# Performance work log

Measured on AMD Instinct MI355X. Metric: run time of the kernel, lower is better.

## Reference

```python
import jax, jax.numpy as jnp
import numpy as np

B, N, D, H = 4, 2048, 512, 8
HD = D // H
SCALE = D ** (-0.5)  # module uses embed_dim**-0.5, not head_dim**-0.5


def setup_inputs() -> dict:
    key = jax.random.key(0)
    k1, k2, k3, k4 = jax.random.split(key, 4)
    x = jax.random.normal(k1, (B, N, D), dtype=jnp.float32)
    # qkv: Linear(D, 3D, bias=False); store as [D, 3D] (x @ W_qkv)
    w_qkv = jax.random.normal(k2, (D, 3 * D), dtype=jnp.float32) * (D ** -0.5)
    # out_proj: Linear(D, D) with bias
    w_out = jax.random.normal(k3, (D, D), dtype=jnp.float32) * (D ** -0.5)
    b_out = jax.random.normal(k4, (D,), dtype=jnp.float32) * 0.01
    return {"x": x, "w_qkv": w_qkv, "w_out": w_out, "b_out": b_out}


def reference(x, w_qkv, w_out, b_out):
    # qkv projection -> [B, N, 3, H, HD] -> split
    qkv = (x @ w_qkv).reshape(B, N, 3, H, HD)
    q = qkv[:, :, 0].transpose(0, 2, 1, 3)  # [B, H, N, HD]
    k = qkv[:, :, 1].transpose(0, 2, 1, 3)
    v = qkv[:, :, 2].transpose(0, 2, 1, 3)
    attn = jnp.einsum("bhqd,bhkd->bhqk", q, k) * SCALE  # [B, H, N, N]
    attn = jax.nn.softmax(attn, axis=-1)
    out = jnp.einsum("bhqk,bhkd->bhqd", attn, v)  # [B, H, N, HD]
    out = out.transpose(0, 2, 1, 3).reshape(B, N, D)
    return out @ w_out + b_out
```

## Files before the change

kernel.cpp:

```cpp
#include <hip/hip_runtime.h>

typedef __attribute__((ext_vector_type(4))) float f32x4;
typedef __attribute__((ext_vector_type(16))) float f32x16;
typedef __attribute__((ext_vector_type(8))) short short8;

#define DEV static __device__ __forceinline__

DEV unsigned short f2bf(float f) {
  union { float f; unsigned u; } x; x.f = f;
  unsigned r = x.u + 0x7fffu + ((x.u >> 16) & 1u);
  return (unsigned short)(r >> 16);
}

DEV float bf2f(unsigned short u) {
  union { unsigned u; float f; } x; x.u = ((unsigned)u) << 16;
  return x.f;
}

DEV f32x4 mfma16(short8 a, short8 b, f32x4 c) {
  return __builtin_amdgcn_mfma_f32_16x16x32_bf16(a, b, c, 0, 0, 0);
}

DEV f32x16 mfma32(short8 a, short8 b, f32x16 c) {
  return __builtin_amdgcn_mfma_f32_32x32x16_bf16(a, b, c, 0, 0, 0);
}

DEV void gload16(const void* g, void* l) {
  __builtin_amdgcn_global_load_lds(
      (const __attribute__((address_space(1))) void*)g,
      (__attribute__((address_space(3))) void*)l, 16, 0, 0);
}

DEV float exp2f_fast(float x) {
  float r;
  asm("v_exp_f32 %0, %1" : "=v"(r) : "v"(x));
  return r;
}

DEV unsigned cvtpk(float lo, float hi) {
  unsigned r;
  asm("v_cvt_pk_bf16_f32 %0, %1, %2" : "=v"(r) : "v"(lo), "v"(hi));
  return r;
}

DEV short8 mk8(unsigned w0, unsigned w1, unsigned w2, unsigned w3) {
  union { unsigned u[4]; short8 s; } x;
  x.u[0] = w0; x.u[1] = w1; x.u[2] = w2; x.u[3] = w3;
  return x.s;
}

DEV int swzrow(int r) { return (((r & 7) ^ ((r >> 3) & 7)) << 3); }

__global__ __launch_bounds__(256) void k_prep(
    const float* __restrict__ x, unsigned short* __restrict__ xb,
    const float* __restrict__ wq, unsigned short* __restrict__ wqT,
    const float* __restrict__ wo, unsigned short* __restrict__ woT) {
  __shared__ unsigned short T[64 * 72];
  const int blk = blockIdx.x;
  const int t = threadIdx.x;
  if (blk < 2048) {
    size_t i = (size_t)blk * 256 + t;
    const f32x4* p = (const f32x4*)(x + i * 8);
    f32x4 a = p[0], b = p[1];
    short8 r;
    r[0] = f2bf(a[0]); r[1] = f2bf(a[1]); r[2] = f2bf(a[2]); r[3] = f2bf(a[3]);
    r[4] = f2bf(b[0]); r[5] = f2bf(b[1]); r[6] = f2bf(b[2]); r[7] = f2bf(b[3]);
    *(short8*)(xb + i * 8) = r;
    return;
  }
  const float* in;
  unsigned short* out;
  int C, bx, by;
  const int R = 512;
  if (blk < 2240) {
    in = wq; out = wqT; C = 1536;
    int bb = blk - 2048; bx = bb % 24; by = bb / 24;
  } else {
    in = wo; out = woT; C = 512;
    int bb = blk - 2240; bx = bb & 7; by = bb >> 3;
  }
  int r0 = by * 64, c0 = bx * 64;
  int rr = t >> 2, seg = t & 3;
  const float* p = in + (size_t)(r0 + rr) * C + c0 + seg * 16;
#pragma unroll
  for (int q = 0; q < 4; ++q) {
    f32x4 v = *(const f32x4*)(p + q * 4);
#pragma unroll
    for (int e = 0; e < 4; ++e) T[rr * 72 + seg * 16 + q * 4 + e] = f2bf(v[e]);
  }
  __syncthreads();
  short8 o0, o1;
#pragma unroll
  for (int e = 0; e < 8; ++e) o0[e] = (short)T[(seg * 16 + e) * 72 + rr];
#pragma unroll
  for (int e = 0; e < 8; ++e) o1[e] = (short)T[(seg * 16 + 8 + e) * 72 + rr];
  unsigned short* q2 = out + (size_t)(c0 + rr) * R + r0 + seg * 16;
  *(short8*)q2 = o0;
  *(short8*)(q2 + 8) = o1;
}

template <bool F32OUT, int NT, bool WVT>
__global__ __launch_bounds__(256) void k_gemm_bt(
    const unsigned short* __restrict__ A, const unsigned short* __restrict__ Bt,
    void* __restrict__ Cp, const float* __restrict__ bias,
    unsigned short* __restrict__ vt, int M, int N, int K) {
  constexpr int NJ = NT / 32;
  constexpr int SHSZ = WVT ? (128 * 136) : (8192 + NT * 64);
  __shared__ unsigned short SH[SHSZ];
  unsigned short* Asm = SH;
  unsigned short* Bsm = SH + 8192;
  const int tid = threadIdx.x;
  const int lane = tid & 63, w = tid >> 6;
  const int wr = w >> 1, wc = w & 1;
  const int nbx = gridDim.x;
  const int cpx = (nbx * gridDim.y) >> 3;
  const int lin = blockIdx.y * nbx + blockIdx.x;
  const int swz = (lin & 7) * cpx + (lin >> 3);
  const int bm = (swz / nbx) * 128, bn = (swz % nbx) * NT;
  const int l15 = lane & 15, l4 = lane >> 4;
  f32x4 acc[4][NJ] = {};
  for (int k0 = 0; k0 < K; k0 += 64) {
    __syncthreads();
#pragma unroll
    for (int j = 0; j < 4; ++j) {
      int c = j * 256 + tid;
      gload16(A + (size_t)(bm + (c >> 3)) * K + k0 + ((c & 7) << 3),
              Asm + (size_t)(j * 256 + w * 64) * 8);
    }
#pragma unroll
    for (int j = 0; j < NJ; ++j) {
      int c = j * 256 + tid;
      gload16(Bt + (size_t)(bn + (c >> 3)) * K + k0 + ((c & 7) << 3),
              Bsm + (size_t)(j * 256 + w * 64) * 8);
    }
    __syncthreads();
#pragma unroll
    for (int kc = 0; kc < 2; ++kc) {
      short8 av[4], bv[NJ];
#pragma unroll
      for (int i = 0; i < 4; ++i)
        av[i] = *(const short8*)&Asm[(wr * 64 + i * 16 + l15) * 64 + kc * 32 + l4 * 8];
#pragma unroll
      for (int j = 0; j < NJ; ++j)
        bv[j] = *(const short8*)&Bsm[(wc * (NT / 2) + j * 16 + l15) * 64 + kc * 32 + l4 * 8];
#pragma unroll
      for (int i = 0; i < 4; ++i)
#pragma unroll
        for (int j = 0; j < NJ; ++j)
          acc[i][j] = mfma16(av[i], bv[j], acc[i][j]);
    }
  }
  if (WVT && bn >= 1024) {
    __syncthreads();
#pragma unroll
    for (int i = 0; i < 4; ++i)
#pragma unroll
      for (int j = 0; j < NJ; ++j) {
        int colL = wc * (NT / 2) + j * 16 + l15;
#pragma unroll
        for (int v = 0; v < 4; ++v)
          SH[colL * 136 + wr * 64 + i * 16 + l4 * 4 + v] = f2bf(acc[i][j][v]);
      }
    __syncthreads();
    const int vtrow = tid >> 1, half2 = tid & 1;
    const int b2 = bm >> 11, npos0 = bm & 2047;
    const int h = ((bn - 1024) >> 6) + (vtrow >> 6);
    const int hd = vtrow & 63;
    unsigned short* dst =
        vt + ((size_t)(b2 * 8 + h) * 64 + hd) * 2048 + npos0 + half2 * 64;
    const unsigned short* srcT = SH + vtrow * 136 + half2 * 64;
#pragma unroll
    for (int e = 0; e < 8; ++e)
      *(short8*)(dst + e * 8) = *(const short8*)(srcT + e * 8);
    return;
  }
#pragma unroll
  for (int i = 0; i < 4; ++i) {
#pragma unroll
    for (int j = 0; j < NJ; ++j) {
      int col = bn + wc * (NT / 2) + j * 16 + l15;
      float bb = 0.f;
      if constexpr (F32OUT) bb = bias[col];
#pragma unroll
      for (int v = 0; v < 4; ++v) {
        int row = bm + wr * 64 + i * 16 + l4 * 4 + v;
        if constexpr (F32OUT) {
          ((float*)Cp)[(size_t)row * N + col] = acc[i][j][v] + bb;
        } else {
          ((unsigned short*)Cp)[(size_t)row * N + col] = f2bf(acc[i][j][v]);
        }
      }
    }
  }
}

__global__ __launch_bounds__(512, 4) void k_attn5(const unsigned short* __restrict__ qkv,
                                                  const unsigned short* __restrict__ vtg,
                                                  unsigned short* __restrict__ O) {
  __shared__ unsigned short smem[16896];
  unsigned short* Ks0 = smem;
  unsigned short* Ks1 = smem + 4096;
  unsigned short* Vs0 = smem + 8192;
  unsigned short* Vs1 = smem + 12288;
  const int tid = threadIdx.x;
  const int lane = tid & 63, w = tid >> 6;
  const int qg = w & 3, half = w >> 2;
  const int l31 = lane & 31, hi = lane >> 5;
  const int bh = blockIdx.y, b = bh >> 3, h = bh & 7;
  const int q0 = blockIdx.x * 128 + qg * 32;
  const float CL = 0.044194173824159216f * 1.4426950408889634f;

  short8 qf[4];
  {
    const unsigned short* qp = qkv + (size_t)(b * 2048 + q0 + l31) * 1536 + h * 64;
#pragma unroll
    for (int ks = 0; ks < 4; ++ks) {
      short8 raw = *(const short8*)(qp + ks * 16 + hi * 8);
      short8 f;
#pragma unroll
      for (int e = 0; e < 8; ++e)
        f[e] = (short)f2bf(bf2f((unsigned short)raw[e]) * CL);
      qf[ks] = f;
    }
  }

  const int sr = tid >> 3, seg = tid & 7;
  const unsigned short* kg = qkv + (size_t)b * 2048 * 1536 + 512 + h * 64 + seg * 8;
  const unsigned short* vg = vtg + (size_t)bh * 64 * 2048 + seg * 8;
  const int so = sr * 64 + ((seg * 8) ^ swzrow(sr));

  *(short8*)&Ks0[so] = *(const short8*)(kg + (size_t)sr * 1536);
  *(short8*)&Vs0[so] = *(const short8*)(vg + (size_t)sr * 2048);
  __syncthreads();

  const int kxor = swzrow(half * 32 + l31);
  const int v0xor = swzrow(l31);
  const int v1xor = swzrow(32 + l31);
  const int krow = (half * 32 + l31) * 64;

  f32x16 oacc0 = {}, oacc1 = {};
  float m_run = 0.f, l_run = 0.f;
  unsigned short* kcur = Ks0; unsigned short* knxt = Ks1;
  unsigned short* vcur = Vs0; unsigned short* vnxt = Vs1;

  for (int t = 0; t < 32; ++t) {
    short8 pk, pv;
    if (t < 31) {
      int kv = (t + 1) * 64;
      pk = *(const short8*)(kg + (size_t)(kv + sr) * 1536);
      pv = *(const short8*)(vg + (size_t)sr * 2048 + kv);
    }

    f32x16 st = {};
    __builtin_amdgcn_s_setprio(1);
#pragma unroll
    for (int ks = 0; ks < 4; ++ks) {
      int col = ks * 16 + hi * 8;
      short8 kf = *(const short8*)&kcur[krow + (col ^ kxor)];
      st = mfma32(kf, qf[ks], st);
    }
    __builtin_amdgcn_s_setprio(0);

    float tm[8];
#pragma unroll
    for (int r = 0; r < 8; ++r) tm[r] = fmaxf(st[r], st[r + 8]);
    float pm = fmaxf(fmaxf(fmaxf(tm[0], tm[1]), fmaxf(tm[2], tm[3])),
                     fmaxf(fmaxf(tm[4], tm[5]), fmaxf(tm[6], tm[7])));
    pm = fmaxf(pm, __shfl_xor(pm, 32));

    if (!__all(pm <= m_run + 11.5f)) {
      float mn = fmaxf(m_run, pm);
      float al = exp2f_fast(m_run - mn);
#pragma unroll
      for (int r = 0; r < 16; ++r) {
        int qd = (r & 3) + 8 * (r >> 2) + 4 * hi;
        float a = __shfl(al, qd);
        oacc0[r] *= a;
        oacc1[r] *= a;
      }
      l_run *= al;
      m_run = mn;
    }

    float p[16];
    float la = 0.f, lb = 0.f;
#pragma unroll
    for (int r = 0; r < 8; ++r) { p[r] = exp2f_fast(st[r] - m_run); la += p[r]; }
#pragma unroll
    for (int r = 8; r < 16; ++r) { p[r] = exp2f_fast(st[r] - m_run); lb += p[r]; }
    float lsum = la + lb;
    short8 pa[2];
#pragma unroll
    for (int g = 0; g < 2; ++g) {
      unsigned pkA0 = cvtpk(p[8 * g + 0], p[8 * g + 1]);
      unsigned pkA1 = cvtpk(p[8 * g + 2], p[8 * g + 3]);
      unsigned pkB0 = cvtpk(p[8 * g + 4], p[8 * g + 5]);
      unsigned pkB1 = cvtpk(p[8 * g + 6], p[8 * g + 7]);
      unsigned tA0 = __shfl_xor(pkA0, 32), tA1 = __shfl_xor(pkA1, 32);
      unsigned tB0 = __shfl_xor(pkB0, 32), tB1 = __shfl_xor(pkB1, 32);
      unsigned w0 = hi ? tB0 : pkA0;
      unsigned w1 = hi ? tB1 : pkA1;
      unsigned w2 = hi ? pkB0 : tA0;
      unsigned w3 = hi ? pkB1 : tA1;
      pa[g] = mk8(w0, w1, w2, w3);
    }
    lsum += __shfl_xor(lsum, 32);
    l_run += lsum;

    __builtin_amdgcn_s_setprio(1);
#pragma unroll
    for (int ks = 0; ks < 2; ++ks) {
      int col = (half * 2 + ks) * 16 + hi * 8;
      short8 vf0 = *(const short8*)&vcur[l31 * 64 + (col ^ v0xor)];
      short8 vf1 = *(const short8*)&vcur[(32 + l31) * 64 + (col ^ v1xor)];
      oacc0 = mfma32(pa[ks], vf0, oacc0);
      oacc1 = mfma32(pa[ks], vf1, oacc1);
    }
    __builtin_amdgcn_s_setprio(0);

    if (t < 31) {
      *(short8*)&knxt[so] = pk;
      *(short8*)&vnxt[so] = pv;
    }
    __syncthreads();
    { unsigned short* tp = kcur; kcur = knxt; knxt = tp; }
    { unsigned short* tp = vcur; vcur = vnxt; vnxt = tp; }
  }

  float* Opart = (float*)smem;
  float* mlbuf = (float*)(smem + 16384);
  if (half == 1) {
    float* op = Opart + qg * 2048;
#pragma unroll
    for (int r = 0; r < 16; ++r) {
      int qd = (r & 3) + 8 * (r >> 2) + 4 * hi;
      op[qd * 64 + l31] = oacc0[r];
      op[qd * 64 + 32 + l31] = oacc1[r];
    }
    if (hi == 0) {
      mlbuf[qg * 64 + l31] = m_run;
      mlbuf[qg * 64 + 32 + l31] = l_run;
    }
  }
  __syncthreads();
  if (half == 0) {
    float mb = mlbuf[qg * 64 + l31];
    float lb2 = mlbuf[qg * 64 + 32 + l31];
    float mmax = fmaxf(m_run, mb);
    float sa = exp2f_fast(m_run - mmax);
    float sb = exp2f_fast(mb - mmax);
    float dI = 1.0f / (l_run * sa + lb2 * sb);
    float fA = sa * dI, fB = sb * dI;
    const float* op = Opart + qg * 2048;
#pragma unroll
    for (int r = 0; r < 16; ++r) {
      int qd = (r & 3) + 8 * (r >> 2) + 4 * hi;
      float fa = __shfl(fA, qd), fb = __shfl(fB, qd);
      float o0 = oacc0[r] * fa + op[qd * 64 + l31] * fb;
      float o1 = oacc1[r] * fa + op[qd * 64 + 32 + l31] * fb;
      size_t row = (size_t)(b * 2048 + q0 + qd) * 512 + h * 64;
      O[row + l31] = f2bf(o0);
      O[row + 32 + l31] = f2bf(o1);
    }
  }
}

extern "C" void kernel_launch(void* const* d_in, const int* in_sizes, int n_in,
                              void* d_out, int out_size, void* d_ws, size_t ws_size,
                              hipStream_t stream) {
  const float* x = (const float*)d_in[0];
  const float* w_qkv = (const float*)d_in[1];
  const float* w_out = (const float*)d_in[2];
  const float* b_out = (const float*)d_in[3];
  float* out = (float*)d_out;
  char* ws = (char*)d_ws;

  unsigned short* xb    = (unsigned short*)(ws + 0);
  unsigned short* wqkvT = (unsigned short*)(ws + 8388608);
  unsigned short* woutT = (unsigned short*)(ws + 9961472);
  unsigned short* qkvb  = (unsigned short*)(ws + 10485760);
  unsigned short* vtb   = (unsigned short*)(ws + 35651584);
  unsigned short* Ob    = (unsigned short*)(ws + 44040192);

  k_prep<<<2304, 256, 0, stream>>>(x, xb, w_qkv, wqkvT, w_out, woutT);
  k_gemm_bt<false, 128, true><<<dim3(12, 64), 256, 0, stream>>>(
      xb, wqkvT, (void*)qkvb, nullptr, vtb, 8192, 1536, 512);
  k_attn5<<<dim3(16, 32), 512, 0, stream>>>(qkvb, vtb, Ob);
  k_gemm_bt<true, 64, false><<<dim3(8, 64), 256, 0, stream>>>(
      Ob, woutT, (void*)out, b_out, nullptr, 8192, 512, 512);
}
```

Baseline: 173.4 us.

## Process two KV tiles per barrier with four-buffer LDS ping-pong in attention

The attention loop now handles two 64-key tiles per iteration, using four K and four V LDS buffers. This halves the number of __syncthreads barriers and issues two tiles' worth of global prefetch at once. LDS read offsets are also precomputed outside the loop. The cost is double the shared memory (about 66KB per block), which may cut the number of resident blocks per CU, plus higher register pressure from the extra prefetch registers.

```diff
diff --git a/kernel.cpp b/kernel.cpp
--- a/kernel.cpp
+++ b/kernel.cpp
@@ -194,14 +194,10 @@
   }
 }
 
-__global__ __launch_bounds__(512, 4) void k_attn5(const unsigned short* __restrict__ qkv,
+__global__ __launch_bounds__(512, 4) void k_attn6(const unsigned short* __restrict__ qkv,
                                                   const unsigned short* __restrict__ vtg,
                                                   unsigned short* __restrict__ O) {
-  __shared__ unsigned short smem[16896];
-  unsigned short* Ks0 = smem;
-  unsigned short* Ks1 = smem + 4096;
-  unsigned short* Vs0 = smem + 8192;
-  unsigned short* Vs1 = smem + 12288;
+  __shared__ unsigned short smem[33792];
   const int tid = threadIdx.x;
   const int lane = tid & 63, w = tid >> 6;
   const int qg = w & 3, half = w >> 2;
@@ -225,38 +221,44 @@
   }
 
   const int sr = tid >> 3, seg = tid & 7;
-  const unsigned short* kg = qkv + (size_t)b * 2048 * 1536 + 512 + h * 64 + seg * 8;
-  const unsigned short* vg = vtg + (size_t)bh * 64 * 2048 + seg * 8;
+  const unsigned short* kg =
+      qkv + (size_t)b * 2048 * 1536 + 512 + h * 64 + (size_t)sr * 1536 + seg * 8;
+  const unsigned short* vg =
+      vtg + (size_t)bh * 64 * 2048 + (size_t)sr * 2048 + seg * 8;
   const int so = sr * 64 + ((seg * 8) ^ swzrow(sr));
 
-  *(short8*)&Ks0[so] = *(const short8*)(kg + (size_t)sr * 1536);
-  *(short8*)&Vs0[so] = *(const short8*)(vg + (size_t)sr * 2048);
+  unsigned short* K0 = smem;          unsigned short* K1 = smem + 4096;
+  unsigned short* K2 = smem + 8192;   unsigned short* K3 = smem + 12288;
+  unsigned short* V0 = smem + 16384;  unsigned short* V1 = smem + 20480;
+  unsigned short* V2 = smem + 24576;  unsigned short* V3 = smem + 28672;
+
+  *(short8*)&K0[so] = *(const short8*)kg;
+  *(short8*)&V0[so] = *(const short8*)vg;
+  *(short8*)&K1[so] = *(const short8*)(kg + 64 * 1536);
+  *(short8*)&V1[so] = *(const short8*)(vg + 64);
   __syncthreads();
 
   const int kxor = swzrow(half * 32 + l31);
-  const int v0xor = swzrow(l31);
-  const int v1xor = swzrow(32 + l31);
   const int krow = (half * 32 + l31) * 64;
+  int kfo[4], vo0[2], vo1[2];
+#pragma unroll
+  for (int ks = 0; ks < 4; ++ks) kfo[ks] = krow + ((ks * 16 + hi * 8) ^ kxor);
+#pragma unroll
+  for (int ks = 0; ks < 2; ++ks) {
+    int col = (half * 2 + ks) * 16 + hi * 8;
+    vo0[ks] = l31 * 64 + (col ^ swzrow(l31));
+    vo1[ks] = (32 + l31) * 64 + (col ^ swzrow(32 + l31));
+  }
 
   f32x16 oacc0 = {}, oacc1 = {};
   float m_run = 0.f, l_run = 0.f;
-  unsigned short* kcur = Ks0; unsigned short* knxt = Ks1;
-  unsigned short* vcur = Vs0; unsigned short* vnxt = Vs1;
-
-  for (int t = 0; t < 32; ++t) {
-    short8 pk, pv;
-    if (t < 31) {
-      int kv = (t + 1) * 64;
-      pk = *(const short8*)(kg + (size_t)(kv + sr) * 1536);
-      pv = *(const short8*)(vg + (size_t)sr * 2048 + kv);
-    }
-
+
+  auto tile = [&](const unsigned short* kb, const unsigned short* vb) {
     f32x16 st = {};
     __builtin_amdgcn_s_setprio(1);
 #pragma unroll
     for (int ks = 0; ks < 4; ++ks) {
-      int col = ks * 16 + hi * 8;
-      short8 kf = *(const short8*)&kcur[krow + (col ^ kxor)];
+      short8 kf = *(const short8*)&kb[kfo[ks]];
       st = mfma32(kf, qf[ks], st);
     }
     __builtin_amdgcn_s_setprio(0);
@@ -310,21 +312,41 @@
     __builtin_amdgcn_s_setprio(1);
 #pragma unroll
     for (int ks = 0; ks < 2; ++ks) {
-      int col = (half * 2 + ks) * 16 + hi * 8;
-      short8 vf0 = *(const short8*)&vcur[l31 * 64 + (col ^ v0xor)];
-      short8 vf1 = *(const short8*)&vcur[(32 + l31) * 64 + (col ^ v1xor)];
+      short8 vf0 = *(const short8*)&vb[vo0[ks]];
+      short8 vf1 = *(const short8*)&vb[vo1[ks]];
       oacc0 = mfma32(pa[ks], vf0, oacc0);
       oacc1 = mfma32(pa[ks], vf1, oacc1);
     }
     __builtin_amdgcn_s_setprio(0);
-
-    if (t < 31) {
-      *(short8*)&knxt[so] = pk;
-      *(short8*)&vnxt[so] = pv;
+  };
+
+  unsigned short *cA = K0, *cB = K1, *sA = K2, *sB = K3;
+  unsigned short *vA = V0, *vB = V1, *wA = V2, *wB = V3;
+  const unsigned short* kgp = kg + 2 * 64 * 1536;
+  const unsigned short* vgp = vg + 2 * 64;
+
+  for (int i = 0; i < 16; ++i) {
+    short8 pk0, pk1, pv0, pv1;
+    const bool more = (i < 15);
+    if (more) {
+      pk0 = *(const short8*)kgp;
+      pk1 = *(const short8*)(kgp + 64 * 1536);
+      pv0 = *(const short8*)vgp;
+      pv1 = *(const short8*)(vgp + 64);
+      kgp += 128 * 1536;
+      vgp += 128;
+    }
+    tile(cA, vA);
+    tile(cB, vB);
+    if (more) {
+      *(short8*)&sA[so] = pk0; *(short8*)&sB[so] = pk1;
+      *(short8*)&wA[so] = pv0; *(short8*)&wB[so] = pv1;
     }
     __syncthreads();
-    { unsigned short* tp = kcur; kcur = knxt; knxt = tp; }
-    { unsigned short* tp = vcur; vcur = vnxt; vnxt = tp; }
+    { unsigned short* t1 = cA; cA = sA; sA = t1; }
+    { unsigned short* t1 = cB; cB = sB; sB = t1; }
+    { unsigned short* t1 = vA; vA = wA; wA = t1; }
+    { unsigned short* t1 = vB; vB = wB; wB = t1; }
   }
 
   float* Opart = (float*)smem;
@@ -385,7 +407,7 @@
   k_prep<<<2304, 256, 0, stream>>>(x, xb, w_qkv, wqkvT, w_out, woutT);
   k_gemm_bt<false, 128, true><<<dim3(12, 64), 256, 0, stream>>>(
       xb, wqkvT, (void*)qkvb, nullptr, vtb, 8192, 1536, 512);
-  k_attn5<<<dim3(16, 32), 512, 0, stream>>>(qkvb, vtb, Ob);
+  k_attn6<<<dim3(16, 32), 512, 0, stream>>>(qkvb, vtb, Ob);
   k_gemm_bt<true, 64, false><<<dim3(8, 64), 256, 0, stream>>>(
       Ob, woutT, (void*)out, b_out, nullptr, 8192, 512, 512);
 }
```

Measured after the change: 176.4 us. No clear change (+1.7%).
